# Kernel tuning notes

Hardware: AMD Instinct MI355X
Metric: run time of the kernel (lower is better)

The kernel has to match this reference:

```python
import jax, jax.numpy as jnp
import numpy as np

B, N, H, Z, C, IN = 4, 32768, 512, 256, 9, 64
N_TRUNK = 4   # fc_2..fc_5
N_HEADS = 4   # xyz, rgb, scale, opacity (n_layers=1 each)
FACTORS = {'xyz': 1.0, 'rgb': 1.0, 'scale': 1.0, 'opacity': 1.0}


def setup_inputs() -> dict:
    key = jax.random.key(0)
    ks = jax.random.split(key, 20)
    rn = lambda k, s, sc=1.0: jax.random.normal(k, s, jnp.float32) * np.float32(sc)
    wg = 1.0 / np.sqrt(H)       # ModLinear weight_gain / sqrt(in_features)
    sg = 1.0 / np.sqrt(Z)       # style-linear init scale
    inp = {
        'pt_feat': rn(ks[0], (B, N, IN)),
        'onehots': jax.random.uniform(ks[1], (B, N, C), jnp.float32),
        'z': rn(ks[2], (B, Z)),
        'fc1_w': rn(ks[3], (H, IN), 1.0 / np.sqrt(IN)),
        'fc1_b': jnp.zeros((H,), jnp.float32),
        'fcma_w': rn(ks[4], (H, C), 1.0 / np.sqrt(C)),
        # stacked ModLinear params: fc_2..fc_5
        'trunk_weight': rn(ks[5], (N_TRUNK, H, H), wg),
        'trunk_walpha': rn(ks[6], (N_TRUNK, H, Z), sg),
        'trunk_balpha': jnp.ones((N_TRUNK, H), jnp.float32),
        'trunk_wbeta': rn(ks[7], (N_TRUNK, H, Z), sg),
        'trunk_bbeta': jnp.zeros((N_TRUNK, H), jnp.float32),
        # stacked ModLinear params: fc_6_{xyz,rgb,scale,opacity}_0
        'head_weight': rn(ks[8], (N_HEADS, H, H), wg),
        'head_walpha': rn(ks[9], (N_HEADS, H, Z), sg),
        'head_balpha': jnp.ones((N_HEADS, H), jnp.float32),
        'head_wbeta': rn(ks[10], (N_HEADS, H, Z), sg),
        'head_bbeta': jnp.zeros((N_HEADS, H), jnp.float32),
        # output heads
        'out_w_xyz': rn(ks[11], (3, H), 1.0 / np.sqrt(H)),
        'out_b_xyz': jnp.zeros((3,), jnp.float32),
        'out_w_rgb': rn(ks[12], (3, H), 1.0 / np.sqrt(H)),
        'out_b_rgb': jnp.zeros((3,), jnp.float32),
        'out_w_scale': rn(ks[13], (3, H), 1.0 / np.sqrt(H)),
        'out_b_scale': jnp.zeros((3,), jnp.float32),
        'out_w_opacity': rn(ks[14], (1, H), 1.0 / np.sqrt(H)),
        'out_b_opacity': jnp.zeros((1,), jnp.float32),
    }
    return inp


def _act(x):
    # LeakyReLU(0.2)
    return jnp.where(x > 0, x, 0.2 * x)


def _modlin(x, z, W, Wa, ba, Wb, bb):
    """ModLinear with bias=False, mod_bias=True, output_mode=True.
    torch: baddbmm(beta, x, (W*alpha).T) == (x*alpha) @ W.T + beta
    x: [B,N,H], z: [B,Z], W: [H,H], Wa/Wb: [H,Z], ba/bb: [H]."""
    alpha = z @ Wa.T + ba            # [B,H] per-batch input scale
    beta = z @ Wb.T + bb             # [B,H] per-batch output bias
    y = jnp.einsum('bni,oi->bno', x * alpha[:, None, :], W)
    return y + beta[:, None, :]


def reference(pt_feat, onehots, z, fc1_w, fc1_b, fcma_w,
              trunk_weight, trunk_walpha, trunk_balpha, trunk_wbeta, trunk_bbeta,
              head_weight, head_walpha, head_balpha, head_wbeta, head_bbeta,
              out_w_xyz, out_b_xyz, out_w_rgb, out_b_rgb,
              out_w_scale, out_b_scale, out_w_opacity, out_b_opacity):
    f = _act(pt_feat @ fc1_w.T + fc1_b + onehots @ fcma_w.T)  # [B,N,H]
    for i in range(N_TRUNK):
        f = _act(_modlin(f, z, trunk_weight[i], trunk_walpha[i], trunk_balpha[i],
                         trunk_wbeta[i], trunk_bbeta[i]))
    heads = [(out_w_xyz, out_b_xyz), (out_w_rgb, out_b_rgb),
             (out_w_scale, out_b_scale), (out_w_opacity, out_b_opacity)]
    outs = []
    for i, (ow, ob) in enumerate(heads):
        g = _act(_modlin(f, z, head_weight[i], head_walpha[i], head_balpha[i],
                         head_wbeta[i], head_bbeta[i]))
        outs.append(g @ ow.T + ob)
    xyz = (jax.nn.sigmoid(outs[0]) - 0.5) * FACTORS['xyz']
    rgb = outs[1] * FACTORS['rgb']
    scale = jnp.clip(outs[2], 1.0, 1.0)
    opacity = jax.nn.sigmoid(outs[3]) * FACTORS['opacity'] + (1.0 - FACTORS['opacity'])
    # concat dict values in fixed key order (xyz,rgb,scale,opacity) -> [B,N,10]
    return jnp.concatenate([xyz, rgb, scale, opacity], axis=-1)
```

## Files before the change

### kernel.cpp

```cpp
#include <hip/hip_runtime.h>
#include <hip/hip_bf16.h>
#include <cstdint>

#define MTOT 131072
#define MC2  65536
#define MCH  32768
#define HDIM 512
#define PLSTR 65600

typedef _Float16 f16x8 __attribute__((ext_vector_type(8)));
typedef _Float16 f16x4 __attribute__((ext_vector_type(4)));
typedef unsigned short u16x8 __attribute__((ext_vector_type(8)));
typedef unsigned short u16x4 __attribute__((ext_vector_type(4)));
typedef float    f32x4 __attribute__((ext_vector_type(4)));

__device__ __forceinline__ float bf2f(unsigned short u) {
  return __uint_as_float(((unsigned)u) << 16);
}

__device__ __forceinline__ float ldin(const void* p, long i, int isbf) {
  if (isbf) return bf2f(((const unsigned short*)p)[i]);
  return ((const float*)p)[i];
}

__device__ __forceinline__ void load_lds16(const void* g, void* lds) {
  __builtin_amdgcn_global_load_lds(
      (const __attribute__((address_space(1))) void*)(unsigned long long)(uintptr_t)g,
      (__attribute__((address_space(3))) void*)(unsigned int)(uintptr_t)lds,
      16, 0, 0);
}

__device__ __forceinline__ float dpp16_sum(float v) {
  int x = __float_as_int(v);
  v += __int_as_float(__builtin_amdgcn_update_dpp(0, x, 0x101, 0xF, 0xF, true));
  x = __float_as_int(v);
  v += __int_as_float(__builtin_amdgcn_update_dpp(0, x, 0x102, 0xF, 0xF, true));
  x = __float_as_int(v);
  v += __int_as_float(__builtin_amdgcn_update_dpp(0, x, 0x104, 0xF, 0xF, true));
  x = __float_as_int(v);
  v += __int_as_float(__builtin_amdgcn_update_dpp(0, x, 0x108, 0xF, 0xF, true));
  return v;
}

__global__ void detect_k(const unsigned* __restrict__ balpha, int* __restrict__ flag) {
  if (threadIdx.x == 0) flag[0] = (balpha[0] == 0x3F803F80u) ? 1 : 0;
}

__global__ __launch_bounds__(256)
void prep_ab(const void* __restrict__ z,
             const void* __restrict__ twa, const void* __restrict__ tba,
             const void* __restrict__ twb, const void* __restrict__ tbb,
             const void* __restrict__ hwa, const void* __restrict__ hba,
             const void* __restrict__ hwb, const void* __restrict__ hbb,
             const int* __restrict__ flag,
             float* __restrict__ alphas, float* __restrict__ betas) {
  const int isbf = flag[0];
  const int bid = blockIdx.x;
  const int og = bid & 7, rest = bid >> 3;
  const int l = rest >> 3, p = (rest >> 2) & 1, b = rest & 3;
  __shared__ float zs[256];
  zs[threadIdx.x] = ldin(z, b * 256 + threadIdx.x, isbf);
  __syncthreads();
  const void *Wsrc, *bsrc;
  long wofs, bofs;
  if (l < 4) {
    Wsrc = (p ? twb : twa); wofs = (long)l * 512 * 256;
    bsrc = (p ? tbb : tba); bofs = l * 512;
  } else {
    const int h = (l == 6) ? 3 : (l - 4);
    Wsrc = (p ? hwb : hwa); wofs = (long)h * 512 * 256;
    bsrc = (p ? hbb : hba); bofs = h * 512;
  }
  const int o = og * 64 + (threadIdx.x >> 2);
  const int kq = threadIdx.x & 3;
  float s = 0.f;
  if (isbf) {
    const unsigned short* wp = (const unsigned short*)Wsrc + wofs + (long)o * 256 + kq * 64;
#pragma unroll
    for (int g = 0; g < 8; g++) {
      u16x8 v = *(const u16x8*)(wp + g * 8);
#pragma unroll
      for (int j = 0; j < 8; j++) s += zs[kq * 64 + g * 8 + j] * bf2f(v[j]);
    }
  } else {
    const float* wp = (const float*)Wsrc + wofs + (long)o * 256 + kq * 64;
#pragma unroll
    for (int g = 0; g < 16; g++) {
      f32x4 v = *(const f32x4*)(wp + g * 4);
#pragma unroll
      for (int j = 0; j < 4; j++) s += zs[kq * 64 + g * 4 + j] * v[j];
    }
  }
  s += __shfl_xor(s, 1, 64);
  s += __shfl_xor(s, 2, 64);
  if (kq == 0) {
    float* dst = (p ? betas : alphas) + (l * 4 + b) * 512;
    dst[o] = s + ldin(bsrc, bofs + o, isbf);
  }
}

__global__ void wmod_k(const void* __restrict__ tw, const void* __restrict__ hw,
                       const int* __restrict__ flag,
                       const float* __restrict__ alphas, _Float16* __restrict__ wmod) {
  const int isbf = flag[0];
  const long t = (long)blockIdx.x * 256 + threadIdx.x;
  const long idx = t * 8;
  const int l   = (int)(idx >> 20);
  const long r0 = idx & ((1 << 20) - 1);
  const int b   = (int)(r0 >> 18);
  const int o   = (int)((r0 >> 9) & 511);
  const int k0  = (int)(r0 & 511);
  const void* wsrc; long ofs;
  if (l < 4) { wsrc = tw; ofs = ((long)l << 18) + (o << 9) + k0; }
  else { const int h = (l == 6) ? 3 : (l - 4); wsrc = hw; ofs = ((long)h << 18) + (o << 9) + k0; }
  const float* al = alphas + (l * 4 + b) * 512 + k0;
  f32x4 a0 = *(const f32x4*)(al);
  f32x4 a1 = *(const f32x4*)(al + 4);
  f16x8 d;
  if (isbf) {
    u16x8 w8 = *(const u16x8*)((const unsigned short*)wsrc + ofs);
#pragma unroll
    for (int j = 0; j < 4; j++) d[j] = (_Float16)(bf2f(w8[j]) * a0[j]);
#pragma unroll
    for (int j = 0; j < 4; j++) d[4 + j] = (_Float16)(bf2f(w8[4 + j]) * a1[j]);
  } else {
    f32x4 w0 = *(const f32x4*)((const float*)wsrc + ofs);
    f32x4 w1 = *(const f32x4*)((const float*)wsrc + ofs + 4);
#pragma unroll
    for (int j = 0; j < 4; j++) d[j] = (_Float16)(w0[j] * a0[j]);
#pragma unroll
    for (int j = 0; j < 4; j++) d[4 + j] = (_Float16)(w1[j] * a1[j]);
  }
  *(f16x8*)(wmod + ((long)(l * 4 + b) << 18) + (o << 9) + k0) = d;
}

__global__ __launch_bounds__(256)
void pack_x(const void* __restrict__ pt, const void* __restrict__ oh,
            long pt_ofs, long oh_ofs, const int* __restrict__ flag,
            _Float16* __restrict__ X) {
  const int isbf = flag[0];
  const int m = blockIdx.x * 8 + (threadIdx.x >> 5);
  const int c5 = threadIdx.x & 31;
  f16x4 d;
  if (c5 < 16) {
    if (isbf) {
      u16x4 v = *(const u16x4*)((const unsigned short*)pt + pt_ofs + (long)m * 64 + c5 * 4);
#pragma unroll
      for (int j = 0; j < 4; j++) d[j] = (_Float16)bf2f(v[j]);
    } else {
      f32x4 v = *(const f32x4*)((const float*)pt + pt_ofs + (long)m * 64 + c5 * 4);
#pragma unroll
      for (int j = 0; j < 4; j++) d[j] = (_Float16)v[j];
    }
  } else {
#pragma unroll
    for (int j = 0; j < 4; j++) {
      const int c = c5 * 4 + j;
      d[j] = (c < 73) ? (_Float16)ldin(oh, oh_ofs + (long)m * 9 + (c - 64), isbf) : (_Float16)0.f;
    }
  }
  *(f16x4*)(X + (long)m * 128 + c5 * 4) = d;
}

__global__ void pack_wc(const void* __restrict__ fc1w, const void* __restrict__ fcmaw,
                        const void* __restrict__ fc1b, const int* __restrict__ flag,
                        _Float16* __restrict__ Wc, float* __restrict__ fb32) {
  const int isbf = flag[0];
  const int o = blockIdx.x, c = threadIdx.x;
  float v = 0.f;
  if (c < 64)      v = ldin(fc1w, o * 64 + c, isbf);
  else if (c < 73) v = ldin(fcmaw, o * 9 + c - 64, isbf);
  Wc[o * 128 + c] = (_Float16)v;
  if (c == 0) fb32[o] = ldin(fc1b, o, isbf);
}

__global__ void conv_small(const void* __restrict__ owx, const void* __restrict__ owr,
                           const void* __restrict__ owo, const void* __restrict__ obx,
                           const void* __restrict__ obr, const void* __restrict__ obo,
                           const int* __restrict__ flag, float* __restrict__ dst) {
  const int t = blockIdx.x * 256 + threadIdx.x;
  if (t >= 3591) return;
  const int isbf = flag[0];
  float v;
  if (t < 1536)      v = ldin(owx, t, isbf);
  else if (t < 3072) v = ldin(owr, t - 1536, isbf);
  else if (t < 3584) v = ldin(owo, t - 3072, isbf);
  else if (t < 3587) v = ldin(obx, t - 3584, isbf);
  else if (t < 3590) v = ldin(obr, t - 3587, isbf);
  else               v = ldin(obo, 0, isbf);
  dst[t] = v;
}

__global__ __launch_bounds__(256)
void gemm_k(const _Float16* __restrict__ A, int lda, int K,
            const _Float16* __restrict__ Wb, int ldb, long wstride,
            const float* __restrict__ biasb, int bstride,
            _Float16* __restrict__ C) {
  __shared__ __align__(16) short As[2 * 128 * 32];
  __shared__ __align__(16) short Bs[2 * 128 * 32];
  const int tid = threadIdx.x;
  const int wave = tid >> 6, lane = tid & 63;
  const int zr = blockIdx.z * MCH;
  const int m0 = blockIdx.x * 128;
  const int n0 = blockIdx.y * 128;
  const _Float16* W = Wb + (long)blockIdx.z * wstride;
  const float* bias = biasb + blockIdx.z * bstride;

  const int l4 = lane >> 2;
  const int sw4 = (lane & 3) ^ (l4 & 3);
  const _Float16* aA = A + (long)(zr + m0 + wave * 32 + l4) * lda + sw4 * 8;
  const _Float16* aB = W + (long)(n0 + wave * 32 + l4) * ldb + sw4 * 8;
  short* dA0 = &As[(wave * 32) * 32];
  short* dA1 = &As[(wave * 32 + 16) * 32];
  short* dB0 = &Bs[(wave * 32) * 32];
  short* dB1 = &Bs[(wave * 32 + 16) * 32];

  const int wm = wave >> 1, wn = wave & 1;
  const int fr = lane & 15, fq = lane >> 4;
  const int sq = (fq ^ (fr & 3)) * 8;

  f32x4 acc[4][4] = {};

  load_lds16(aA, dA0);
  load_lds16(aA + 16 * (long)lda, dA1);
  load_lds16(aB, dB0);
  load_lds16(aB + 16 * (long)ldb, dB1);

  const int nIter = K >> 5;
  for (int k = 0; k < nIter; k++) {
    const int cur = (k & 1) << 12;
    __syncthreads();
    if (k + 1 < nIter) {
      const int nxt = ((k + 1) & 1) << 12;
      const long ko = (long)(k + 1) * 32;
      load_lds16(aA + ko, dA0 + nxt);
      load_lds16(aA + ko + 16 * (long)lda, dA1 + nxt);
      load_lds16(aB + ko, dB0 + nxt);
      load_lds16(aB + ko + 16 * (long)ldb, dB1 + nxt);
    }
    f16x8 af[4], bfv[4];
#pragma unroll
    for (int i = 0; i < 4; i++)
      af[i] = *(const f16x8*)&As[cur + (wm * 64 + i * 16 + fr) * 32 + sq];
#pragma unroll
    for (int j = 0; j < 4; j++)
      bfv[j] = *(const f16x8*)&Bs[cur + (wn * 64 + j * 16 + fr) * 32 + sq];
#pragma unroll
    for (int i = 0; i < 4; i++)
#pragma unroll
      for (int j = 0; j < 4; j++)
        acc[i][j] = __builtin_amdgcn_mfma_f32_16x16x32_f16(af[i], bfv[j], acc[i][j], 0, 0, 0);
  }

#pragma unroll
  for (int j = 0; j < 4; j++) {
    const int col = n0 + wn * 64 + j * 16 + fr;
    const float bv = bias[col];
#pragma unroll
    for (int i = 0; i < 4; i++) {
      const long row = (long)zr + m0 + wm * 64 + i * 16 + fq * 4;
#pragma unroll
      for (int r = 0; r < 4; r++) {
        float v = acc[i][j][r] + bv;
        v = v > 0.f ? v : 0.2f * v;
        C[(row + r) * HDIM + col] = (_Float16)v;
      }
    }
  }
}

#define BAR() asm volatile("s_barrier" ::: "memory")
#define VMC(n) asm volatile("s_waitcnt vmcnt(" #n ")" ::: "memory")
#define LGK0() do { asm volatile("s_waitcnt lgkmcnt(0)" ::: "memory"); \
                    __builtin_amdgcn_sched_barrier(0); } while (0)
#define PR1 __builtin_amdgcn_s_setprio(1)
#define PR0 __builtin_amdgcn_s_setprio(0)

template <int NOUT, int CBASE>
__global__ __launch_bounds__(512, 2)
void gemm256_t(const _Float16* __restrict__ A,
               const _Float16* __restrict__ Wb, long wstride,
               const float* __restrict__ biasb, int bstride,
               _Float16* __restrict__ C,
               const float* __restrict__ P,
               float* __restrict__ part) {
  __shared__ __align__(16) short As[2][16384];
  __shared__ __align__(16) short Bs[2][16384];
  const int tid = threadIdx.x;
  const int wave = tid >> 6, lane = tid & 63;
  const int gsw = (blockIdx.x & 7) * 64 + (blockIdx.x >> 3);
  const int z = gsw >> 8;
  const int n0 = (gsw & 1) * 256;
  const int m0 = ((gsw >> 1) & 127) * 256;
  const long zr = (long)z * MCH;
  const _Float16* W = Wb + (long)z * wstride;
  const float* bias = biasb + z * bstride;

  const int srow = lane >> 3;
  const int schk = (lane & 7) ^ srow;
  const _Float16* gA = A + (zr + m0 + wave * 8 + srow) * 512L + schk * 8;
  const _Float16* gB = W + ((long)(n0 + wave * 8 + srow)) * 512L + schk * 8;
  short* lA = &As[0][0] + wave * 512;
  short* lB = &Bs[0][0] + wave * 512;

#define STGA(buf, t, j) load_lds16(gA + (t) * 64 + (j) * (64 * 512L), lA + (buf) * 16384 + (j) * 4096)
#define STGB(buf, t, j) load_lds16(gB + (t) * 64 + (j) * (64 * 512L), lB + (buf) * 16384 + (j) * 4096)

  const int fr = lane & 15, fq = lane >> 4;
  const int wm = wave >> 2, wn = wave & 3;
  const int c0 = (fq ^ (fr & 7)) * 8;
  const int c1 = c0 ^ 32;
  const int aB0 = (wm * 128 + fr) * 64;
  const int bB0 = (wn * 64 + fr) * 64;

  f16x8 aLo[4][2], aHi[4][2], bLo[2][2], bHi[2][2];
  f32x4 acc[8][4] = {};

#define RDAL(buf, i) { aLo[i][0] = *(const f16x8*)&As[buf][aB0 + (i) * 1024 + c0]; \
                       aLo[i][1] = *(const f16x8*)&As[buf][aB0 + (i) * 1024 + c1]; }
#define RDAH(buf, i) { aHi[i][0] = *(const f16x8*)&As[buf][aB0 + ((i) + 4) * 1024 + c0]; \
                       aHi[i][1] = *(const f16x8*)&As[buf][aB0 + ((i) + 4) * 1024 + c1]; }
#define RDBL(buf, j) { bLo[j][0] = *(const f16x8*)&Bs[buf][bB0 + (j) * 1024 + c0]; \
                       bLo[j][1] = *(const f16x8*)&Bs[buf][bB0 + (j) * 1024 + c1]; }
#define RDBH(buf, j) { bHi[j][0] = *(const f16x8*)&Bs[buf][bB0 + ((j) + 2) * 1024 + c0]; \
                       bHi[j][1] = *(const f16x8*)&Bs[buf][bB0 + ((j) + 2) * 1024 + c1]; }
#define MMQ(AF, io, BF, jo) { \
  _Pragma("unroll") for (int il = 0; il < 4; il++) \
  _Pragma("unroll") for (int jl = 0; jl < 2; jl++) { \
    acc[(io) + il][(jo) + jl] = __builtin_amdgcn_mfma_f32_16x16x32_f16( \
        AF[il][0], BF[jl][0], acc[(io) + il][(jo) + jl], 0, 0, 0); \
    acc[(io) + il][(jo) + jl] = __builtin_amdgcn_mfma_f32_16x16x32_f16( \
        AF[il][1], BF[jl][1], acc[(io) + il][(jo) + jl], 0, 0, 0); } }

  STGB(0, 0, 0); STGB(0, 0, 1); STGB(0, 0, 2); STGB(0, 0, 3);
  STGA(0, 0, 0); STGA(0, 0, 1); STGA(0, 0, 2); STGA(0, 0, 3);
  STGB(1, 1, 0); STGB(1, 1, 1); STGB(1, 1, 2); STGB(1, 1, 3);
  STGA(1, 1, 0); STGA(1, 1, 1); STGA(1, 1, 2); STGA(1, 1, 3);
  VMC(8); BAR();

#pragma unroll
  for (int t = 0; t < 8; t++) {
    const int buf = t & 1;
    RDAL(buf, 0) RDAL(buf, 1) RDAL(buf, 2) RDAL(buf, 3)
    RDBL(buf, 0) RDBL(buf, 1)
    RDBH(buf, 0) RDBH(buf, 1)
    RDAH(buf, 0) RDAH(buf, 1) RDAH(buf, 2) RDAH(buf, 3)
    PR1; MMQ(aLo, 0, bLo, 0); MMQ(aLo, 0, bHi, 2); PR0;
    LGK0();
    BAR();
    if (t + 2 < 8) { STGB(buf, t + 2, 0); STGB(buf, t + 2, 1);
                     STGB(buf, t + 2, 2); STGB(buf, t + 2, 3);
                     STGA(buf, t + 2, 0); STGA(buf, t + 2, 1);
                     STGA(buf, t + 2, 2); STGA(buf, t + 2, 3); }
    PR1; MMQ(aHi, 4, bLo, 0); MMQ(aHi, 4, bHi, 2); PR0;
    if (t < 6) { VMC(8); } else if (t == 6) { VMC(0); }
    BAR();
  }

  float bv[4];
#pragma unroll
  for (int j = 0; j < 4; j++) bv[j] = bias[n0 + wn * 64 + j * 16 + fr];

  if constexpr (NOUT == 0) {
#pragma unroll
    for (int i = 0; i < 8; i++) {
      const long row = zr + m0 + wm * 128 + i * 16 + fq * 4;
#pragma unroll
      for (int r = 0; r < 4; r++) {
        _Float16* cp = C + (row + r) * HDIM + n0 + wn * 64 + fr;
#pragma unroll
        for (int j = 0; j < 4; j++) {
          float v = acc[i][j][r] + bv[j];
          v = v > 0.f ? v : 0.2f * v;
          cp[j * 16] = (_Float16)v;
        }
      }
    }
  } else {
    const int slot = ((n0 >> 8) << 2) + wn;
#pragma unroll
    for (int i = 0; i < 8; i++) {
#pragma unroll
      for (int r = 0; r < 4; r++) {
        const long row = zr + m0 + wm * 128 + i * 16 + fq * 4 + r;
        float av[4];
#pragma unroll
        for (int j = 0; j < 4; j++) {
          float v = acc[i][j][r] + bv[j];
          av[j] = v > 0.f ? v : 0.2f * v;
        }
#pragma unroll
        for (int c = 0; c < NOUT; c++) {
          const float* Pc = P + c * 512 + n0 + wn * 64 + fr;
          float s = av[0] * Pc[0] + av[1] * Pc[16] + av[2] * Pc[32] + av[3] * Pc[48];
          s = dpp16_sum(s);
          if (fr == 0) part[(long)((CBASE + c) * 8 + slot) * PLSTR + row] = s;
        }
      }
    }
  }
#undef STGA
#undef STGB
#undef RDAL
#undef RDAH
#undef RDBL
#undef RDBH
#undef MMQ
}

__global__ __launch_bounds__(256)
void fin_k(const float* __restrict__ part, const float* __restrict__ ob,
           const int* __restrict__ flag, void* __restrict__ outv, long row0) {
  const long row = (long)blockIdx.x * 256 + threadIdx.x;
  float s[7];
#pragma unroll
  for (int c = 0; c < 7; c++) {
    float acc = 0.f;
#pragma unroll
    for (int sl = 0; sl < 8; sl++) acc += part[(long)(c * 8 + sl) * PLSTR + row];
    s[c] = acc;
  }
  float v[10];
#pragma unroll
  for (int c = 0; c < 3; c++) v[c] = 1.f / (1.f + __expf(-(s[c] + ob[c]))) - 0.5f;
#pragma unroll
  for (int c = 0; c < 3; c++) v[3 + c] = s[3 + c] + ob[3 + c];
  v[6] = 1.0f; v[7] = 1.0f; v[8] = 1.0f;
  v[9] = 1.f / (1.f + __expf(-(s[6] + ob[6])));
  const long ro = (row0 + row) * 10;
  if (flag[0]) {
    __hip_bfloat16* o = (__hip_bfloat16*)outv + ro;
#pragma unroll
    for (int c = 0; c < 10; c++) o[c] = __float2bfloat16(v[c]);
  } else {
    float* o = (float*)outv + ro;
#pragma unroll
    for (int c = 0; c < 10; c++) o[c] = v[c];
  }
}

extern "C" void kernel_launch(void* const* d_in, const int* in_sizes, int n_in,
                              void* d_out, int out_size, void* d_ws, size_t ws_size,
                              hipStream_t stream) {
  const void* pt    = d_in[0];
  const void* oh    = d_in[1];
  const void* z     = d_in[2];
  const void* fc1w  = d_in[3];
  const void* fc1b  = d_in[4];
  const void* fcmaw = d_in[5];
  const void* tw    = d_in[6];
  const void* twa   = d_in[7];
  const void* tba   = d_in[8];
  const void* twb   = d_in[9];
  const void* tbb   = d_in[10];
  const void* hw    = d_in[11];
  const void* hwa   = d_in[12];
  const void* hba   = d_in[13];
  const void* hwb   = d_in[14];
  const void* hbb   = d_in[15];
  const void* owx   = d_in[16];
  const void* obx   = d_in[17];
  const void* owr   = d_in[18];
  const void* obr   = d_in[19];
  const void* owo   = d_in[22];
  const void* obo   = d_in[23];

  char* ws = (char*)d_ws;
  _Float16* g0    = (_Float16*)(ws + 0);
  _Float16* g1    = (_Float16*)(ws + 67108864LL);
  _Float16* X     = (_Float16*)(ws + 67108864LL);
  _Float16* wmodp = (_Float16*)(ws + 134217728LL);
  _Float16* Wc    = (_Float16*)(ws + 148897792LL);
  float* alphas   = (float*)(ws + 149028864LL);
  float* betas    = (float*)(ws + 149086208LL);
  float* fb32     = (float*)(ws + 149143552LL);
  int*   dflag    = (int*)  (ws + 149145600LL);
  float* ow32     = (float*)(ws + 149145664LL);
  float* part     = (float*)(ws + 167772160LL);

  detect_k<<<1, 64, 0, stream>>>((const unsigned*)tba, dflag);
  prep_ab<<<448, 256, 0, stream>>>(z, twa, tba, twb, tbb, hwa, hba, hwb, hbb, dflag, alphas, betas);
  wmod_k<<<3584, 256, 0, stream>>>(tw, hw, dflag, alphas, wmodp);
  pack_wc<<<512, 128, 0, stream>>>(fc1w, fcmaw, fc1b, dflag, Wc, fb32);
  conv_small<<<15, 256, 0, stream>>>(owx, owr, owo, obx, obr, obo, dflag, ow32);

  dim3 gg(MCH / 128, 4, 2), gb(256);
  for (int p = 0; p < 2; p++) {
    const long prow = (long)p * MC2;
    pack_x<<<MC2 / 8, 256, 0, stream>>>(pt, oh, prow * 64, prow * 9, dflag, X);
    gemm_k<<<gg, gb, 0, stream>>>(X, 128, 128, Wc, 128, 0, fb32, 0, g0);
    _Float16* fin = g0; _Float16* fout = g1;
    for (int l = 0; l < 4; l++) {
      gemm256_t<0, 0><<<512, 512, 0, stream>>>(fin, wmodp + (long)(l * 4 + p * 2) * 262144, 262144,
                                               betas + (l * 4 + p * 2) * 512, 512, fout,
                                               nullptr, nullptr);
      _Float16* t = fin; fin = fout; fout = t;
    }
    gemm256_t<3, 0><<<512, 512, 0, stream>>>(fin, wmodp + (long)(4 * 4 + p * 2) * 262144, 262144,
                                             betas + (4 * 4 + p * 2) * 512, 512, nullptr,
                                             ow32, part);
    gemm256_t<3, 3><<<512, 512, 0, stream>>>(fin, wmodp + (long)(5 * 4 + p * 2) * 262144, 262144,
                                             betas + (5 * 4 + p * 2) * 512, 512, nullptr,
                                             ow32 + 1536, part);
    gemm256_t<1, 6><<<512, 512, 0, stream>>>(fin, wmodp + (long)(6 * 4 + p * 2) * 262144, 262144,
                                             betas + (6 * 4 + p * 2) * 512, 512, nullptr,
                                             ow32 + 3072, part);
    fin_k<<<MC2 / 256, 256, 0, stream>>>(part, ow32 + 3584, dflag, d_out, prow);
  }
}
```

Before: 830.1 us.

## Shrink GEMM tile to 256x128 with K=32 steps for higher occupancy

The main modulated-linear GEMM kernel changes from 256x256 output tiles with K=64 stages to 256x128 tiles with K=32 stages. The LDS footprint drops sharply and launch bounds allow 4 blocks per CU, with twice as many blocks launched. The LDS swizzle, wave layout, fragment reads and head partial-slot mapping are rebuilt to match. This trades per-tile data reuse and arithmetic intensity for more occupancy and latency hiding, and it doubles the number of barriers and pipeline steps along K.

```diff
diff --git a/kernel.cpp b/kernel.cpp
--- a/kernel.cpp
+++ b/kernel.cpp
@@ -277,83 +277,71 @@
 #define PR0 __builtin_amdgcn_s_setprio(0)
 
 template <int NOUT, int CBASE>
-__global__ __launch_bounds__(512, 2)
+__global__ __launch_bounds__(512, 4)
 void gemm256_t(const _Float16* __restrict__ A,
                const _Float16* __restrict__ Wb, long wstride,
                const float* __restrict__ biasb, int bstride,
                _Float16* __restrict__ C,
                const float* __restrict__ P,
                float* __restrict__ part) {
-  __shared__ __align__(16) short As[2][16384];
-  __shared__ __align__(16) short Bs[2][16384];
+  __shared__ __align__(16) short As[2][8192];
+  __shared__ __align__(16) short Bs[2][4096];
   const int tid = threadIdx.x;
   const int wave = tid >> 6, lane = tid & 63;
-  const int gsw = (blockIdx.x & 7) * 64 + (blockIdx.x >> 3);
-  const int z = gsw >> 8;
-  const int n0 = (gsw & 1) * 256;
-  const int m0 = ((gsw >> 1) & 127) * 256;
+  const int gsw = (blockIdx.x & 7) * 128 + (blockIdx.x >> 3);
+  const int z = gsw >> 9;
+  const int rest = gsw & 511;
+  const int nt = rest & 3;
+  const int n0 = nt * 128;
+  const int m0 = (rest >> 2) * 256;
   const long zr = (long)z * MCH;
   const _Float16* W = Wb + (long)z * wstride;
   const float* bias = biasb + z * bstride;
 
-  const int srow = lane >> 3;
-  const int schk = (lane & 7) ^ srow;
-  const _Float16* gA = A + (zr + m0 + wave * 8 + srow) * 512L + schk * 8;
-  const _Float16* gB = W + ((long)(n0 + wave * 8 + srow)) * 512L + schk * 8;
-  short* lA = &As[0][0] + wave * 512;
+  const int srow = lane >> 2;
+  const int schk = (lane & 3) ^ ((srow >> 1) & 3);
+  const _Float16* gA = A + (zr + m0 + wave * 32 + srow) * 512L + schk * 8;
+  const _Float16* gB = W + ((long)(n0 + wave * 16 + srow)) * 512L + schk * 8;
+  short* lA = &As[0][0] + wave * 1024;
   short* lB = &Bs[0][0] + wave * 512;
 
-#define STGA(buf, t, j) load_lds16(gA + (t) * 64 + (j) * (64 * 512L), lA + (buf) * 16384 + (j) * 4096)
-#define STGB(buf, t, j) load_lds16(gB + (t) * 64 + (j) * (64 * 512L), lB + (buf) * 16384 + (j) * 4096)
+#define STGA(buf, t, j) load_lds16(gA + (t) * 32 + (j) * (16 * 512L), lA + (buf) * 8192 + (j) * 512)
+#define STGB(buf, t)    load_lds16(gB + (t) * 32, lB + (buf) * 4096)
 
   const int fr = lane & 15, fq = lane >> 4;
-  const int wm = wave >> 2, wn = wave & 3;
-  const int c0 = (fq ^ (fr & 7)) * 8;
-  const int c1 = c0 ^ 32;
-  const int aB0 = (wm * 128 + fr) * 64;
-  const int bB0 = (wn * 64 + fr) * 64;
-
-  f16x8 aLo[4][2], aHi[4][2], bLo[2][2], bHi[2][2];
-  f32x4 acc[8][4] = {};
-
-#define RDAL(buf, i) { aLo[i][0] = *(const f16x8*)&As[buf][aB0 + (i) * 1024 + c0]; \
-                       aLo[i][1] = *(const f16x8*)&As[buf][aB0 + (i) * 1024 + c1]; }
-#define RDAH(buf, i) { aHi[i][0] = *(const f16x8*)&As[buf][aB0 + ((i) + 4) * 1024 + c0]; \
-                       aHi[i][1] = *(const f16x8*)&As[buf][aB0 + ((i) + 4) * 1024 + c1]; }
-#define RDBL(buf, j) { bLo[j][0] = *(const f16x8*)&Bs[buf][bB0 + (j) * 1024 + c0]; \
-                       bLo[j][1] = *(const f16x8*)&Bs[buf][bB0 + (j) * 1024 + c1]; }
-#define RDBH(buf, j) { bHi[j][0] = *(const f16x8*)&Bs[buf][bB0 + ((j) + 2) * 1024 + c0]; \
-                       bHi[j][1] = *(const f16x8*)&Bs[buf][bB0 + ((j) + 2) * 1024 + c1]; }
-#define MMQ(AF, io, BF, jo) { \
-  _Pragma("unroll") for (int il = 0; il < 4; il++) \
-  _Pragma("unroll") for (int jl = 0; jl < 2; jl++) { \
-    acc[(io) + il][(jo) + jl] = __builtin_amdgcn_mfma_f32_16x16x32_f16( \
-        AF[il][0], BF[jl][0], acc[(io) + il][(jo) + jl], 0, 0, 0); \
-    acc[(io) + il][(jo) + jl] = __builtin_amdgcn_mfma_f32_16x16x32_f16( \
-        AF[il][1], BF[jl][1], acc[(io) + il][(jo) + jl], 0, 0, 0); } }
-
-  STGB(0, 0, 0); STGB(0, 0, 1); STGB(0, 0, 2); STGB(0, 0, 3);
-  STGA(0, 0, 0); STGA(0, 0, 1); STGA(0, 0, 2); STGA(0, 0, 3);
-  STGB(1, 1, 0); STGB(1, 1, 1); STGB(1, 1, 2); STGB(1, 1, 3);
-  STGA(1, 1, 0); STGA(1, 1, 1); STGA(1, 1, 2); STGA(1, 1, 3);
-  VMC(8); BAR();
-
-#pragma unroll
-  for (int t = 0; t < 8; t++) {
+  const int wm = wave >> 1, wn = wave & 1;
+  const int cks = (fq ^ ((fr >> 1) & 3)) * 8;
+  const int aB0 = (wm * 64 + fr) * 32;
+  const int bB0 = (wn * 64 + fr) * 32;
+
+  f16x8 aF[4], bF[4];
+  f32x4 acc[4][4] = {};
+
+#define RDA(buf, i) { aF[i] = *(const f16x8*)&As[buf][aB0 + (i) * 512 + cks]; }
+#define RDB(buf, j) { bF[j] = *(const f16x8*)&Bs[buf][bB0 + (j) * 512 + cks]; }
+#define MM(i, j) acc[i][j] = __builtin_amdgcn_mfma_f32_16x16x32_f16(aF[i], bF[j], acc[i][j], 0, 0, 0);
+
+  STGA(0, 0, 0); STGA(0, 0, 1); STGB(0, 0);
+  STGA(1, 1, 0); STGA(1, 1, 1); STGB(1, 1);
+  VMC(3); BAR();
+
+#pragma unroll
+  for (int t = 0; t < 16; t++) {
     const int buf = t & 1;
-    RDAL(buf, 0) RDAL(buf, 1) RDAL(buf, 2) RDAL(buf, 3)
-    RDBL(buf, 0) RDBL(buf, 1)
-    RDBH(buf, 0) RDBH(buf, 1)
-    RDAH(buf, 0) RDAH(buf, 1) RDAH(buf, 2) RDAH(buf, 3)
-    PR1; MMQ(aLo, 0, bLo, 0); MMQ(aLo, 0, bHi, 2); PR0;
+    RDA(buf, 0) RDA(buf, 1) RDA(buf, 2) RDA(buf, 3)
+    RDB(buf, 0) RDB(buf, 1) RDB(buf, 2) RDB(buf, 3)
+    PR1;
+    MM(0, 0) MM(0, 1) MM(0, 2) MM(0, 3)
+    MM(1, 0) MM(1, 1) MM(1, 2) MM(1, 3)
+    PR0;
     LGK0();
     BAR();
-    if (t + 2 < 8) { STGB(buf, t + 2, 0); STGB(buf, t + 2, 1);
-                     STGB(buf, t + 2, 2); STGB(buf, t + 2, 3);
-                     STGA(buf, t + 2, 0); STGA(buf, t + 2, 1);
-                     STGA(buf, t + 2, 2); STGA(buf, t + 2, 3); }
-    PR1; MMQ(aHi, 4, bLo, 0); MMQ(aHi, 4, bHi, 2); PR0;
-    if (t < 6) { VMC(8); } else if (t == 6) { VMC(0); }
+    if (t + 2 < 16) { STGA(buf, t + 2, 0); STGA(buf, t + 2, 1); STGB(buf, t + 2); }
+    PR1;
+    MM(2, 0) MM(2, 1) MM(2, 2) MM(2, 3)
+    MM(3, 0) MM(3, 1) MM(3, 2) MM(3, 3)
+    PR0;
+    if (t < 14) { VMC(3); } else if (t == 14) { VMC(0); }
     BAR();
   }
 
@@ -363,8 +351,8 @@
 
   if constexpr (NOUT == 0) {
 #pragma unroll
-    for (int i = 0; i < 8; i++) {
-      const long row = zr + m0 + wm * 128 + i * 16 + fq * 4;
+    for (int i = 0; i < 4; i++) {
+      const long row = zr + m0 + wm * 64 + i * 16 + fq * 4;
 #pragma unroll
       for (int r = 0; r < 4; r++) {
         _Float16* cp = C + (row + r) * HDIM + n0 + wn * 64 + fr;
@@ -377,12 +365,12 @@
       }
     }
   } else {
-    const int slot = ((n0 >> 8) << 2) + wn;
-#pragma unroll
-    for (int i = 0; i < 8; i++) {
+    const int slot = nt * 2 + wn;
+#pragma unroll
+    for (int i = 0; i < 4; i++) {
 #pragma unroll
       for (int r = 0; r < 4; r++) {
-        const long row = zr + m0 + wm * 128 + i * 16 + fq * 4 + r;
+        const long row = zr + m0 + wm * 64 + i * 16 + fq * 4 + r;
         float av[4];
 #pragma unroll
         for (int j = 0; j < 4; j++) {
@@ -401,11 +389,9 @@
   }
 #undef STGA
 #undef STGB
-#undef RDAL
-#undef RDAH
-#undef RDBL
-#undef RDBH
-#undef MMQ
+#undef RDA
+#undef RDB
+#undef MM
 }
 
 __global__ __launch_bounds__(256)
@@ -491,20 +477,20 @@
     gemm_k<<<gg, gb, 0, stream>>>(X, 128, 128, Wc, 128, 0, fb32, 0, g0);
     _Float16* fin = g0; _Float16* fout = g1;
     for (int l = 0; l < 4; l++) {
-      gemm256_t<0, 0><<<512, 512, 0, stream>>>(fin, wmodp + (long)(l * 4 + p * 2) * 262144, 262144,
-                                               betas + (l * 4 + p * 2) * 512, 512, fout,
-                                               nullptr, nullptr);
+      gemm256_t<0, 0><<<1024, 512, 0, stream>>>(fin, wmodp + (long)(l * 4 + p * 2) * 262144, 262144,
+                                                betas + (l * 4 + p * 2) * 512, 512, fout,
+                                                nullptr, nullptr);
       _Float16* t = fin; fin = fout; fout = t;
     }
-    gemm256_t<3, 0><<<512, 512, 0, stream>>>(fin, wmodp + (long)(4 * 4 + p * 2) * 262144, 262144,
-                                             betas + (4 * 4 + p * 2) * 512, 512, nullptr,
-                                             ow32, part);
-    gemm256_t<3, 3><<<512, 512, 0, stream>>>(fin, wmodp + (long)(5 * 4 + p * 2) * 262144, 262144,
-                                             betas + (5 * 4 + p * 2) * 512, 512, nullptr,
-                                             ow32 + 1536, part);
-    gemm256_t<1, 6><<<512, 512, 0, stream>>>(fin, wmodp + (long)(6 * 4 + p * 2) * 262144, 262144,
-                                             betas + (6 * 4 + p * 2) * 512, 512, nullptr,
-                                             ow32 + 3072, part);
+    gemm256_t<3, 0><<<1024, 512, 0, stream>>>(fin, wmodp + (long)(4 * 4 + p * 2) * 262144, 262144,
+                                              betas + (4 * 4 + p * 2) * 512, 512, nullptr,
+                                              ow32, part);
+    gemm256_t<3, 3><<<1024, 512, 0, stream>>>(fin, wmodp + (long)(5 * 4 + p * 2) * 262144, 262144,
+                                              betas + (5 * 4 + p * 2) * 512, 512, nullptr,
+                                              ow32 + 1536, part);
+    gemm256_t<1, 6><<<1024, 512, 0, stream>>>(fin, wmodp + (long)(6 * 4 + p * 2) * 262144, 262144,
+                                              betas + (6 * 4 + p * 2) * 512, 512, nullptr,
+                                              ow32 + 3072, part);
     fin_k<<<MC2 / 256, 256, 0, stream>>>(part, ow32 + 3584, dflag, d_out, prow);
   }
 }
```

New measurement: 862.4 us. 1.04x slower.
